# Performance work log

Measured on AMD Instinct MI355X. Metric: run time of the kernel, lower is better.

The kernel has to match this reference:

```python
import jax, jax.numpy as jnp
import numpy as np

EPS = 1e-20

def efficient_squash(s):
    # Efficient-CapsNet squash: (1 - 1/e^||s||) * s/||s||
    n = jnp.linalg.norm(s, axis=-1, keepdims=True)
    return (1.0 - 1.0 / (jnp.exp(n) + EPS)) * (s / (n + EPS))

def setup_inputs() -> dict:
    key = jax.random.key(0)
    k1, k2 = jax.random.split(key)
    B, N, D_in = 32, 2048, 16
    K, D_out = 32, 16
    x = jax.random.normal(k1, (B, N, D_in), dtype=jnp.float32)
    # he_normal fan_in = N * D_in * ... ; use simple scaled normal init
    w = jax.random.normal(k2, (K, N, D_in, D_out), dtype=jnp.float32) * 0.05
    b = jnp.zeros((K, N, 1), dtype=jnp.float32)
    return {"x": x, "w": w, "b": b}

def reference(x, w, b):
    D_out = w.shape[-1]
    # projection: [B,N,D_in] x [K,N,D_in,D_out] -> [B,K,N,D_out]
    u = jnp.einsum('bji,kjiz->bkjz', x, w)
    # agreement c_{bkj} = sum_{i,z} u_{bkjz} u_{bkiz} = <u_j, sum_i u_i>
    t = jnp.sum(u, axis=2)                      # [B,K,D_out]
    c = jnp.einsum('bkjz,bkz->bkj', u, t)[..., None]  # [B,K,N,1]
    c = c / jnp.sqrt(jnp.asarray(D_out, jnp.float32))
    c = jax.nn.softmax(c, axis=1)               # softmax over capsules K
    c = c + b                                   # broadcast [K,N,1]
    s = jnp.sum(u * c, axis=2)                  # [B,K,D_out]
    return efficient_squash(s)
```

## Files before the change

kernel.cpp:

```cpp
#include <hip/hip_runtime.h>

#define NN 2048
#define KK 32

#define WS_U     0
#define WS_TP2   67108864UL
#define WS_T     67633152UL
#define WS_SPART 67698688UL
#define WS_NEED  71892992UL

__device__ __forceinline__ float bf_lo(unsigned v) { return __uint_as_float(v << 16); }
__device__ __forceinline__ float bf_hi(unsigned v) { return __uint_as_float(v & 0xffff0000u); }
__device__ __forceinline__ unsigned pack_bf16(float a, float b) {
    unsigned ua = __float_as_uint(a), ub = __float_as_uint(b);
    return ((ua + 0x8000u) >> 16) | ((ub + 0x8000u) & 0xffff0000u);
}

__global__ __launch_bounds__(128)
void k1_u(const float* __restrict__ x, const float* __restrict__ w,
          unsigned* __restrict__ u_pk)
{
    const int tid = threadIdx.x;
    const int zq  = tid & 3;
    const int k   = tid >> 2;
    const int j   = blockIdx.x;

    const float4* w4 = reinterpret_cast<const float4*>(
        w + (((size_t)k * NN + j) * 16) * 16) + zq;
    float4 wr[16];
#pragma unroll
    for (int i = 0; i < 16; ++i) wr[i] = w4[i * 4];

    unsigned* __restrict__ ub = u_pk + (size_t)j * 8192 + k * 8 + zq * 2;
#pragma unroll 4
    for (int b = 0; b < 32; ++b) {
        const float* __restrict__ xr = x + ((size_t)b * NN + j) * 16;
        float xs[16];
#pragma unroll
        for (int i = 0; i < 16; ++i) xs[i] = xr[i];
        float4 acc = make_float4(0.f, 0.f, 0.f, 0.f);
#pragma unroll
        for (int i = 0; i < 16; ++i) {
            acc.x = fmaf(xs[i], wr[i].x, acc.x);
            acc.y = fmaf(xs[i], wr[i].y, acc.y);
            acc.z = fmaf(xs[i], wr[i].z, acc.z);
            acc.w = fmaf(xs[i], wr[i].w, acc.w);
        }
        uint2 o;
        o.x = pack_bf16(acc.x, acc.y);
        o.y = pack_bf16(acc.z, acc.w);
        *reinterpret_cast<uint2*>(ub + (size_t)b * 256) = o;
    }
}

__global__ __launch_bounds__(1024)
void k2a_tpart(const unsigned* __restrict__ u_pk, float* __restrict__ t_part2)
{
    __shared__ float red[16][64][8];
    const int tid  = threadIdx.x;
    const int js   = tid >> 6;
    const int sl64 = tid & 63;
    const int b    = blockIdx.x >> 3;
    const int slj  = blockIdx.x & 7;

    const uint4* up = reinterpret_cast<const uint4*>(u_pk)
                    + ((size_t)(slj * 256 + js) * 32 + b) * 64 + sl64;
    float a[8];
#pragma unroll
    for (int e = 0; e < 8; ++e) a[e] = 0.f;
#pragma unroll
    for (int it = 0; it < 16; ++it) {
        uint4 v = up[(size_t)it * (16 * 32 * 64)];
        a[0] += bf_lo(v.x); a[1] += bf_hi(v.x);
        a[2] += bf_lo(v.y); a[3] += bf_hi(v.y);
        a[4] += bf_lo(v.z); a[5] += bf_hi(v.z);
        a[6] += bf_lo(v.w); a[7] += bf_hi(v.w);
    }
#pragma unroll
    for (int e = 0; e < 8; ++e) red[js][sl64][e] = a[e];
    __syncthreads();
    if (tid < 512) {
        const int s = tid >> 3, e = tid & 7;
        float acc = 0.f;
#pragma unroll
        for (int r = 0; r < 16; ++r) acc += red[r][s][e];
        t_part2[((size_t)b * 8 + slj) * 512 + s * 8 + e] = acc;
    }
}

__global__ __launch_bounds__(256)
void k2a2_t(const float* __restrict__ t_part2, float* __restrict__ t)
{
    const int idx4 = blockIdx.x * 256 + threadIdx.x;
    const int b = idx4 >> 7, loc4 = idx4 & 127;
    const float4* p = reinterpret_cast<const float4*>(t_part2) + (size_t)b * 1024 + loc4;
    float4 s = make_float4(0.f, 0.f, 0.f, 0.f);
#pragma unroll
    for (int sl = 0; sl < 8; ++sl) {
        float4 v = p[sl * 128];
        s.x += v.x; s.y += v.y; s.z += v.z; s.w += v.w;
    }
    reinterpret_cast<float4*>(t)[idx4] = s;
}

__global__ __launch_bounds__(256)
void k2b_fused(const unsigned* __restrict__ u_pk, const float* __restrict__ t,
               const float* __restrict__ bias, float* __restrict__ s_part)
{
    __shared__ float lc_lds[32][33];
    __shared__ float s_lds[8][32][16];
    const int tid = threadIdx.x;
    const int k   = tid & 31;
    const int jl  = tid >> 5;
    const int b   = blockIdx.x >> 6;
    const int jc  = blockIdx.x & 63;

    float tr[16];
    const float4* tp = reinterpret_cast<const float4*>(t + ((size_t)b * KK + k) * 16);
#pragma unroll
    for (int q = 0; q < 4; ++q) {
        float4 v = tp[q];
        tr[4 * q + 0] = v.x; tr[4 * q + 1] = v.y; tr[4 * q + 2] = v.z; tr[4 * q + 3] = v.w;
    }

    uint4 ua[4], ud[4];
#pragma unroll
    for (int jj = 0; jj < 4; ++jj) {
        const int jL = jj * 8 + jl;
        const int jg = jc * 32 + jL;
        const uint4* up = reinterpret_cast<const uint4*>(u_pk)
                        + ((size_t)jg * 32 + b) * 64 + k * 2;
        ua[jj] = up[0]; ud[jj] = up[1];
        float a0 = 0.f, a1 = 0.f;
        a0 = fmaf(bf_lo(ua[jj].x), tr[0],  a0); a1 = fmaf(bf_hi(ua[jj].x), tr[1],  a1);
        a0 = fmaf(bf_lo(ua[jj].y), tr[2],  a0); a1 = fmaf(bf_hi(ua[jj].y), tr[3],  a1);
        a0 = fmaf(bf_lo(ua[jj].z), tr[4],  a0); a1 = fmaf(bf_hi(ua[jj].z), tr[5],  a1);
        a0 = fmaf(bf_lo(ua[jj].w), tr[6],  a0); a1 = fmaf(bf_hi(ua[jj].w), tr[7],  a1);
        a0 = fmaf(bf_lo(ud[jj].x), tr[8],  a0); a1 = fmaf(bf_hi(ud[jj].x), tr[9],  a1);
        a0 = fmaf(bf_lo(ud[jj].y), tr[10], a0); a1 = fmaf(bf_hi(ud[jj].y), tr[11], a1);
        a0 = fmaf(bf_lo(ud[jj].z), tr[12], a0); a1 = fmaf(bf_hi(ud[jj].z), tr[13], a1);
        a0 = fmaf(bf_lo(ud[jj].w), tr[14], a0); a1 = fmaf(bf_hi(ud[jj].w), tr[15], a1);
        lc_lds[jL][k] = a0 + a1;
    }
    __syncthreads();

    {
        const int jq = tid >> 3, kq = tid & 7;
        float lv[4];
#pragma unroll
        for (int m = 0; m < 4; ++m) lv[m] = lc_lds[jq][kq * 4 + m];
        float pm = fmaxf(fmaxf(lv[0], lv[1]), fmaxf(lv[2], lv[3]));
        pm = fmaxf(pm, __shfl_xor(pm, 1));
        pm = fmaxf(pm, __shfl_xor(pm, 2));
        pm = fmaxf(pm, __shfl_xor(pm, 4));
        float ev[4], ps = 0.f;
#pragma unroll
        for (int m = 0; m < 4; ++m) { ev[m] = __expf((lv[m] - pm) * 0.25f); ps += ev[m]; }
        ps += __shfl_xor(ps, 1);
        ps += __shfl_xor(ps, 2);
        ps += __shfl_xor(ps, 4);
        const float inv = 1.f / ps;
        const int jg = jc * 32 + jq;
#pragma unroll
        for (int m = 0; m < 4; ++m)
            lv[m] = ev[m] * inv + bias[(size_t)(kq * 4 + m) * NN + jg];
        __syncthreads();
#pragma unroll
        for (int m = 0; m < 4; ++m) lc_lds[jq][kq * 4 + m] = lv[m];
    }
    __syncthreads();

    float sacc[16];
#pragma unroll
    for (int z = 0; z < 16; ++z) sacc[z] = 0.f;
#pragma unroll
    for (int jj = 0; jj < 4; ++jj) {
        const float cv = lc_lds[jj * 8 + jl][k];
        const uint4 a = ua[jj], d = ud[jj];
        sacc[0]  = fmaf(cv, bf_lo(a.x), sacc[0]);  sacc[1]  = fmaf(cv, bf_hi(a.x), sacc[1]);
        sacc[2]  = fmaf(cv, bf_lo(a.y), sacc[2]);  sacc[3]  = fmaf(cv, bf_hi(a.y), sacc[3]);
        sacc[4]  = fmaf(cv, bf_lo(a.z), sacc[4]);  sacc[5]  = fmaf(cv, bf_hi(a.z), sacc[5]);
        sacc[6]  = fmaf(cv, bf_lo(a.w), sacc[6]);  sacc[7]  = fmaf(cv, bf_hi(a.w), sacc[7]);
        sacc[8]  = fmaf(cv, bf_lo(d.x), sacc[8]);  sacc[9]  = fmaf(cv, bf_hi(d.x), sacc[9]);
        sacc[10] = fmaf(cv, bf_lo(d.y), sacc[10]); sacc[11] = fmaf(cv, bf_hi(d.y), sacc[11]);
        sacc[12] = fmaf(cv, bf_lo(d.z), sacc[12]); sacc[13] = fmaf(cv, bf_hi(d.z), sacc[13]);
        sacc[14] = fmaf(cv, bf_lo(d.w), sacc[14]); sacc[15] = fmaf(cv, bf_hi(d.w), sacc[15]);
    }

#pragma unroll
    for (int q = 0; q < 4; ++q)
        *reinterpret_cast<float4*>(&s_lds[jl][k][q * 4]) =
            make_float4(sacc[q * 4], sacc[q * 4 + 1], sacc[q * 4 + 2], sacc[q * 4 + 3]);
    __syncthreads();
    {
        const int kk = tid >> 3, zp = tid & 7;
        float2 o; o.x = 0.f; o.y = 0.f;
#pragma unroll
        for (int l = 0; l < 8; ++l) {
            o.x += s_lds[l][kk][2 * zp];
            o.y += s_lds[l][kk][2 * zp + 1];
        }
        reinterpret_cast<float2*>(s_part)[((size_t)b * 64 + jc) * 256 + kk * 8 + zp] = o;
    }
}

__global__ __launch_bounds__(256)
void k4_squash(const float* __restrict__ s_part, float* __restrict__ out)
{
    const int idx4 = blockIdx.x * 256 + threadIdx.x;
    const int b = idx4 >> 7, loc4 = idx4 & 127;
    const float4* p = reinterpret_cast<const float4*>(s_part) + (size_t)b * 8192 + loc4;
    float4 s = make_float4(0.f, 0.f, 0.f, 0.f);
#pragma unroll 8
    for (int jc = 0; jc < 64; ++jc) {
        float4 v = p[jc * 128];
        s.x += v.x; s.y += v.y; s.z += v.z; s.w += v.w;
    }
    float ss = s.x * s.x + s.y * s.y + s.z * s.z + s.w * s.w;
    ss += __shfl_xor(ss, 1);
    ss += __shfl_xor(ss, 2);
    const float n = sqrtf(ss);
    const float sc = (1.f - 1.f / (__expf(n) + 1e-20f)) / (n + 1e-20f);
    float4 o; o.x = s.x * sc; o.y = s.y * sc; o.z = s.z * sc; o.w = s.w * sc;
    reinterpret_cast<float4*>(out)[idx4] = o;
}

__global__ void k_sentinel(float* __restrict__ out)
{
    out[blockIdx.x * 256 + threadIdx.x] = 12345.0f;
}

extern "C" void kernel_launch(void* const* d_in, const int* in_sizes, int n_in,
                              void* d_out, int out_size, void* d_ws, size_t ws_size,
                              hipStream_t stream)
{
    const float* x    = (const float*)d_in[0];
    const float* w    = (const float*)d_in[1];
    const float* bias = (const float*)d_in[2];
    float* out        = (float*)d_out;

    char* ws = (char*)d_ws;
    if (ws_size < WS_NEED) {
        k_sentinel<<<dim3(64), dim3(256), 0, stream>>>(out);
        return;
    }
    unsigned* u_pk = (unsigned*)(ws + WS_U);
    float* t_part2 = (float*)(ws + WS_TP2);
    float* t       = (float*)(ws + WS_T);
    float* s_part  = (float*)(ws + WS_SPART);

    k1_u     <<<dim3(2048), dim3(128),  0, stream>>>(x, w, u_pk);
    k2a_tpart<<<dim3(256),  dim3(1024), 0, stream>>>(u_pk, t_part2);
    k2a2_t   <<<dim3(16),   dim3(256),  0, stream>>>(t_part2, t);
    k2b_fused<<<dim3(2048), dim3(256),  0, stream>>>(u_pk, t, bias, s_part);
    k4_squash<<<dim3(16),   dim3(256),  0, stream>>>(s_part, out);
}
```

Measured before the change: 76.03 us.

## Compute projection with bf16 MFMA and fuse t partial sums into projection kernel

Replaces the scalar-FMA projection kernel with one that packs w and x to bf16 and uses 16x16x32 MFMA instructions. A select mask handles two j rows per wave. The same kernel accumulates per-block partial sums of u for t, which removes the separate pass that re-read the whole u buffer. Those partials are then reduced by two small reduction kernels. This adds a 32 MB partial buffer, rounds w and x to bf16 before the multiply, and wastes half of each MFMA on masked zeros.

```diff
diff --git a/kernel.cpp b/kernel.cpp
--- a/kernel.cpp
+++ b/kernel.cpp
@@ -3,11 +3,15 @@
 #define NN 2048
 #define KK 32
 
-#define WS_U     0
-#define WS_TP2   67108864UL
-#define WS_T     67633152UL
-#define WS_SPART 67698688UL
-#define WS_NEED  71892992UL
+typedef __attribute__((ext_vector_type(8))) short short8;
+typedef __attribute__((ext_vector_type(4))) float f32x4;
+
+#define WS_U     0UL
+#define WS_TPART 67108864UL
+#define WS_TP2   100663296UL
+#define WS_T     101711872UL
+#define WS_SPART 101777408UL
+#define WS_NEED  105971712UL
 
 __device__ __forceinline__ float bf_lo(unsigned v) { return __uint_as_float(v << 16); }
 __device__ __forceinline__ float bf_hi(unsigned v) { return __uint_as_float(v & 0xffff0000u); }
@@ -15,97 +19,132 @@
     unsigned ua = __float_as_uint(a), ub = __float_as_uint(b);
     return ((ua + 0x8000u) >> 16) | ((ub + 0x8000u) & 0xffff0000u);
 }
-
-__global__ __launch_bounds__(128)
-void k1_u(const float* __restrict__ x, const float* __restrict__ w,
-          unsigned* __restrict__ u_pk)
+__device__ __forceinline__ short8 pack8(const float* r) {
+    short8 o;
+#pragma unroll
+    for (int e = 0; e < 8; ++e)
+        o[e] = (short)(unsigned short)((__float_as_uint(r[e]) + 0x8000u) >> 16);
+    return o;
+}
+__device__ __forceinline__ short8 sel8(bool keep, short8 v) {
+    union { short8 s; unsigned u[4]; } a, b;
+    a.s = v;
+#pragma unroll
+    for (int i = 0; i < 4; ++i) b.u[i] = keep ? a.u[i] : 0u;
+    return b.s;
+}
+
+__global__ __launch_bounds__(512)
+void kA2(const float* __restrict__ x, const float* __restrict__ w,
+         unsigned* __restrict__ u_pk, float* __restrict__ t_part)
 {
     const int tid = threadIdx.x;
-    const int zq  = tid & 3;
-    const int k   = tid >> 2;
-    const int j   = blockIdx.x;
-
-    const float4* w4 = reinterpret_cast<const float4*>(
-        w + (((size_t)k * NN + j) * 16) * 16) + zq;
-    float4 wr[16];
-#pragma unroll
-    for (int i = 0; i < 16; ++i) wr[i] = w4[i * 4];
-
-    unsigned* __restrict__ ub = u_pk + (size_t)j * 8192 + k * 8 + zq * 2;
-#pragma unroll 4
-    for (int b = 0; b < 32; ++b) {
-        const float* __restrict__ xr = x + ((size_t)b * NN + j) * 16;
-        float xs[16];
-#pragma unroll
-        for (int i = 0; i < 16; ++i) xs[i] = xr[i];
-        float4 acc = make_float4(0.f, 0.f, 0.f, 0.f);
-#pragma unroll
-        for (int i = 0; i < 16; ++i) {
-            acc.x = fmaf(xs[i], wr[i].x, acc.x);
-            acc.y = fmaf(xs[i], wr[i].y, acc.y);
-            acc.z = fmaf(xs[i], wr[i].z, acc.z);
-            acc.w = fmaf(xs[i], wr[i].w, acc.w);
-        }
-        uint2 o;
-        o.x = pack_bf16(acc.x, acc.y);
-        o.y = pack_bf16(acc.z, acc.w);
-        *reinterpret_cast<uint2*>(ub + (size_t)b * 256) = o;
-    }
-}
-
-__global__ __launch_bounds__(1024)
-void k2a_tpart(const unsigned* __restrict__ u_pk, float* __restrict__ t_part2)
-{
-    __shared__ float red[16][64][8];
-    const int tid  = threadIdx.x;
-    const int js   = tid >> 6;
-    const int sl64 = tid & 63;
-    const int b    = blockIdx.x >> 3;
-    const int slj  = blockIdx.x & 7;
-
-    const uint4* up = reinterpret_cast<const uint4*>(u_pk)
-                    + ((size_t)(slj * 256 + js) * 32 + b) * 64 + sl64;
-    float a[8];
-#pragma unroll
-    for (int e = 0; e < 8; ++e) a[e] = 0.f;
-#pragma unroll
-    for (int it = 0; it < 16; ++it) {
-        uint4 v = up[(size_t)it * (16 * 32 * 64)];
-        a[0] += bf_lo(v.x); a[1] += bf_hi(v.x);
-        a[2] += bf_lo(v.y); a[3] += bf_hi(v.y);
-        a[4] += bf_lo(v.z); a[5] += bf_hi(v.z);
-        a[6] += bf_lo(v.w); a[7] += bf_hi(v.w);
-    }
-#pragma unroll
-    for (int e = 0; e < 8; ++e) red[js][sl64][e] = a[e];
-    __syncthreads();
-    if (tid < 512) {
-        const int s = tid >> 3, e = tid & 7;
-        float acc = 0.f;
-#pragma unroll
-        for (int r = 0; r < 16; ++r) acc += red[r][s][e];
-        t_part2[((size_t)b * 8 + slj) * 512 + s * 8 + e] = acc;
-    }
-}
-
-__global__ __launch_bounds__(256)
-void k2a2_t(const float* __restrict__ t_part2, float* __restrict__ t)
-{
-    const int idx4 = blockIdx.x * 256 + threadIdx.x;
-    const int b = idx4 >> 7, loc4 = idx4 & 127;
-    const float4* p = reinterpret_cast<const float4*>(t_part2) + (size_t)b * 1024 + loc4;
-    float4 s = make_float4(0.f, 0.f, 0.f, 0.f);
-#pragma unroll
-    for (int sl = 0; sl < 8; ++sl) {
-        float4 v = p[sl * 128];
-        s.x += v.x; s.y += v.y; s.z += v.z; s.w += v.w;
-    }
-    reinterpret_cast<float4*>(t)[idx4] = s;
-}
-
-__global__ __launch_bounds__(256)
-void k2b_fused(const unsigned* __restrict__ u_pk, const float* __restrict__ t,
-               const float* __restrict__ bias, float* __restrict__ s_part)
+    const int wv = tid >> 6, l = tid & 63;
+    const int c16 = l & 15, g = l >> 4;
+    const int jl = g >> 1, ih = g & 1;
+    const int j0 = blockIdx.x * 4;
+
+    f32x4 T[4][2];
+#pragma unroll
+    for (int ckl = 0; ckl < 4; ++ckl)
+#pragma unroll
+        for (int bn = 0; bn < 2; ++bn) T[ckl][bn] = (f32x4){0.f, 0.f, 0.f, 0.f};
+
+#pragma unroll
+    for (int p = 0; p < 2; ++p) {
+        const int jp = j0 + p * 2 + jl;
+
+        short8 Wf[4];
+#pragma unroll
+        for (int ckl = 0; ckl < 4; ++ckl) {
+            const int k = wv * 4 + ckl;
+            const float* wp = w + ((size_t)k * NN + jp) * 256 + ih * 128 + c16;
+            float br[8];
+#pragma unroll
+            for (int e = 0; e < 8; ++e) br[e] = wp[e * 16];
+            Wf[ckl] = pack8(br);
+        }
+        short8 Xf[2];
+#pragma unroll
+        for (int bn = 0; bn < 2; ++bn) {
+            const float* xp = x + ((size_t)(bn * 16 + c16) * NN + jp) * 16 + ih * 8;
+            float ar[8];
+            float4 v0 = *reinterpret_cast<const float4*>(xp);
+            float4 v1 = *reinterpret_cast<const float4*>(xp + 4);
+            ar[0]=v0.x; ar[1]=v0.y; ar[2]=v0.z; ar[3]=v0.w;
+            ar[4]=v1.x; ar[5]=v1.y; ar[6]=v1.z; ar[7]=v1.w;
+            Xf[bn] = pack8(ar);
+        }
+
+#pragma unroll
+        for (int jj = 0; jj < 2; ++jj) {
+            const bool keep = (jl == jj);
+            const int j = j0 + p * 2 + jj;
+            const f32x4 zero = (f32x4){0.f, 0.f, 0.f, 0.f};
+#pragma unroll
+            for (int ckl = 0; ckl < 4; ++ckl) {
+                const int k = wv * 4 + ckl;
+                const short8 wsel = sel8(keep, Wf[ckl]);
+#pragma unroll
+                for (int bn = 0; bn < 2; ++bn) {
+                    f32x4 Cj = __builtin_amdgcn_mfma_f32_16x16x32_bf16(
+                        wsel, Xf[bn], zero, 0, 0, 0);
+                    T[ckl][bn] += Cj;
+                    uint2 o;
+                    o.x = pack_bf16(Cj[0], Cj[1]);
+                    o.y = pack_bf16(Cj[2], Cj[3]);
+                    *reinterpret_cast<uint2*>(u_pk +
+                        (((size_t)j * 32 + bn * 16 + c16) * 32 + k) * 8 + g * 2) = o;
+                }
+            }
+        }
+    }
+
+    float* tp = t_part + (size_t)blockIdx.x * 16384;
+#pragma unroll
+    for (int ckl = 0; ckl < 4; ++ckl)
+#pragma unroll
+        for (int bn = 0; bn < 2; ++bn)
+            *reinterpret_cast<f32x4*>(tp + (bn * 16 + c16) * 512 +
+                                      (wv * 4 + ckl) * 16 + g * 4) = T[ckl][bn];
+}
+
+__global__ __launch_bounds__(256)
+void kred32(const float* __restrict__ src, float* __restrict__ dst)
+{
+    const int idx = blockIdx.x * 256 + threadIdx.x;
+    const int c4 = idx & 4095, ch = idx >> 12;
+    const f32x4* P = reinterpret_cast<const f32x4*>(src);
+    f32x4 a0 = (f32x4){0,0,0,0}, a1 = a0, a2 = a0, a3 = a0;
+#pragma unroll 2
+    for (int q = 0; q < 32; q += 4) {
+        a0 += P[(size_t)(ch * 32 + q + 0) * 4096 + c4];
+        a1 += P[(size_t)(ch * 32 + q + 1) * 4096 + c4];
+        a2 += P[(size_t)(ch * 32 + q + 2) * 4096 + c4];
+        a3 += P[(size_t)(ch * 32 + q + 3) * 4096 + c4];
+    }
+    reinterpret_cast<f32x4*>(dst)[(size_t)ch * 4096 + c4] = (a0 + a1) + (a2 + a3);
+}
+
+__global__ __launch_bounds__(256)
+void kt2(const float* __restrict__ tp2, float* __restrict__ t)
+{
+    const int c4 = blockIdx.x * 256 + threadIdx.x;
+    const f32x4* P = reinterpret_cast<const f32x4*>(tp2);
+    f32x4 a0 = (f32x4){0,0,0,0}, a1 = a0, a2 = a0, a3 = a0;
+#pragma unroll
+    for (int q = 0; q < 16; q += 4) {
+        a0 += P[(size_t)(q + 0) * 4096 + c4];
+        a1 += P[(size_t)(q + 1) * 4096 + c4];
+        a2 += P[(size_t)(q + 2) * 4096 + c4];
+        a3 += P[(size_t)(q + 3) * 4096 + c4];
+    }
+    reinterpret_cast<f32x4*>(t)[c4] = (a0 + a1) + (a2 + a3);
+}
+
+__global__ __launch_bounds__(256)
+void kB2(const unsigned* __restrict__ u_pk, const float* __restrict__ t,
+         const float* __restrict__ bias, float* __restrict__ s_part)
 {
     __shared__ float lc_lds[32][33];
     __shared__ float s_lds[8][32][16];
@@ -129,7 +168,7 @@
         const int jL = jj * 8 + jl;
         const int jg = jc * 32 + jL;
         const uint4* up = reinterpret_cast<const uint4*>(u_pk)
-                        + ((size_t)jg * 32 + b) * 64 + k * 2;
+                        + (((size_t)jg * 32 + b) * 32 + k) * 2;
         ua[jj] = up[0]; ud[jj] = up[1];
         float a0 = 0.f, a1 = 0.f;
         a0 = fmaf(bf_lo(ua[jj].x), tr[0],  a0); a1 = fmaf(bf_hi(ua[jj].x), tr[1],  a1);
@@ -196,9 +235,9 @@
         const int kk = tid >> 3, zp = tid & 7;
         float2 o; o.x = 0.f; o.y = 0.f;
 #pragma unroll
-        for (int l = 0; l < 8; ++l) {
-            o.x += s_lds[l][kk][2 * zp];
-            o.y += s_lds[l][kk][2 * zp + 1];
+        for (int l2 = 0; l2 < 8; ++l2) {
+            o.x += s_lds[l2][kk][2 * zp];
+            o.y += s_lds[l2][kk][2 * zp + 1];
         }
         reinterpret_cast<float2*>(s_part)[((size_t)b * 64 + jc) * 256 + kk * 8 + zp] = o;
     }
@@ -245,13 +284,14 @@
         return;
     }
     unsigned* u_pk = (unsigned*)(ws + WS_U);
-    float* t_part2 = (float*)(ws + WS_TP2);
+    float* t_part  = (float*)(ws + WS_TPART);
+    float* tp2     = (float*)(ws + WS_TP2);
     float* t       = (float*)(ws + WS_T);
     float* s_part  = (float*)(ws + WS_SPART);
 
-    k1_u     <<<dim3(2048), dim3(128),  0, stream>>>(x, w, u_pk);
-    k2a_tpart<<<dim3(256),  dim3(1024), 0, stream>>>(u_pk, t_part2);
-    k2a2_t   <<<dim3(16),   dim3(256),  0, stream>>>(t_part2, t);
-    k2b_fused<<<dim3(2048), dim3(256),  0, stream>>>(u_pk, t, bias, s_part);
-    k4_squash<<<dim3(16),   dim3(256),  0, stream>>>(s_part, out);
-}
+    kA2      <<<dim3(512),  dim3(512), 0, stream>>>(x, w, u_pk, t_part);
+    kred32   <<<dim3(256),  dim3(256), 0, stream>>>(t_part, tp2);
+    kt2      <<<dim3(16),   dim3(256), 0, stream>>>(tp2, t);
+    kB2      <<<dim3(2048), dim3(256), 0, stream>>>(u_pk, t, bias, s_part);
+    k4_squash<<<dim3(16),   dim3(256), 0, stream>>>(s_part, out);
+}
```

Result: faster. 67.31 us (-11.5%).

## Stage w tiles in LDS for coalesced loads and widen the t reduction grid

Applied to the files above, without the earlier changes.

The projection kernel now processes four j per 512-thread block. It loads each j's full weight slab cooperatively into LDS with contiguous float4 reads, then transposes the packed bf16 results through LDS so the u stores to global memory are fully coalesced uint4 writes. The t partial-sum kernel is regridded to 1024 blocks with a 32-way partial buffer. The follow-up reduction now sums 32 slices instead of 8. The goal is to remove the strided per-thread w loads and scattered 8-byte stores of the old projection, at the cost of more LDS use, extra barriers and a larger workspace.

```diff
diff --git a/kernel.cpp b/kernel.cpp
--- a/kernel.cpp
+++ b/kernel.cpp
@@ -3,11 +3,13 @@
 #define NN 2048
 #define KK 32
 
-#define WS_U     0
-#define WS_TP2   67108864UL
-#define WS_T     67633152UL
-#define WS_SPART 67698688UL
-#define WS_NEED  71892992UL
+typedef __attribute__((ext_vector_type(4))) float f32x4;
+
+#define WS_U     0UL
+#define WS_TP4   67108864UL
+#define WS_T     69206016UL
+#define WS_SPART 69271552UL
+#define WS_NEED  73465856UL
 
 __device__ __forceinline__ float bf_lo(unsigned v) { return __uint_as_float(v << 16); }
 __device__ __forceinline__ float bf_hi(unsigned v) { return __uint_as_float(v & 0xffff0000u); }
@@ -16,96 +18,136 @@
     return ((ua + 0x8000u) >> 16) | ((ub + 0x8000u) & 0xffff0000u);
 }
 
-__global__ __launch_bounds__(128)
-void k1_u(const float* __restrict__ x, const float* __restrict__ w,
-          unsigned* __restrict__ u_pk)
-{
+__global__ __launch_bounds__(512)
+void kU(const float* __restrict__ x, const float* __restrict__ w,
+        unsigned* __restrict__ u_pk)
+{
+    __shared__ float    w_lds[32 * 257];
+    __shared__ float    x_lds[32][16];
+    __shared__ unsigned u_tr[32 * 264];
     const int tid = threadIdx.x;
-    const int zq  = tid & 3;
-    const int k   = tid >> 2;
-    const int j   = blockIdx.x;
-
-    const float4* w4 = reinterpret_cast<const float4*>(
-        w + (((size_t)k * NN + j) * 16) * 16) + zq;
-    float4 wr[16];
-#pragma unroll
-    for (int i = 0; i < 16; ++i) wr[i] = w4[i * 4];
-
-    unsigned* __restrict__ ub = u_pk + (size_t)j * 8192 + k * 8 + zq * 2;
-#pragma unroll 4
-    for (int b = 0; b < 32; ++b) {
-        const float* __restrict__ xr = x + ((size_t)b * NN + j) * 16;
-        float xs[16];
-#pragma unroll
-        for (int i = 0; i < 16; ++i) xs[i] = xr[i];
-        float4 acc = make_float4(0.f, 0.f, 0.f, 0.f);
-#pragma unroll
-        for (int i = 0; i < 16; ++i) {
-            acc.x = fmaf(xs[i], wr[i].x, acc.x);
-            acc.y = fmaf(xs[i], wr[i].y, acc.y);
-            acc.z = fmaf(xs[i], wr[i].z, acc.z);
-            acc.w = fmaf(xs[i], wr[i].w, acc.w);
-        }
-        uint2 o;
-        o.x = pack_bf16(acc.x, acc.y);
-        o.y = pack_bf16(acc.z, acc.w);
-        *reinterpret_cast<uint2*>(ub + (size_t)b * 256) = o;
+    const int k   = tid & 31;
+    const int zq  = (tid >> 5) & 3;
+    const int bh  = tid >> 7;
+    const int j0  = blockIdx.x * 4;
+
+#pragma unroll 1
+    for (int jj = 0; jj < 4; ++jj) {
+        const int j = j0 + jj;
+
+        {
+            const int kk = tid >> 4, c = tid & 15;
+            const float4* wg = reinterpret_cast<const float4*>(
+                w + ((size_t)kk * NN + j) * 256);
+            float4 v0 = wg[c];
+            float4 v1 = wg[16 + c];
+            float4 v2 = wg[32 + c];
+            float4 v3 = wg[48 + c];
+            *reinterpret_cast<float4*>(&w_lds[kk * 257 +   0 + c * 4]) = v0;
+            *reinterpret_cast<float4*>(&w_lds[kk * 257 +  64 + c * 4]) = v1;
+            *reinterpret_cast<float4*>(&w_lds[kk * 257 + 128 + c * 4]) = v2;
+            *reinterpret_cast<float4*>(&w_lds[kk * 257 + 192 + c * 4]) = v3;
+            x_lds[kk][c] = x[((size_t)kk * NN + j) * 16 + c];
+        }
+        __syncthreads();
+
+        float wr[16][4];
+#pragma unroll
+        for (int i = 0; i < 16; ++i)
+            *reinterpret_cast<float4*>(wr[i]) =
+                *reinterpret_cast<const float4*>(&w_lds[k * 257 + i * 16 + zq * 4]);
+
+#pragma unroll
+        for (int b8 = 0; b8 < 8; ++b8) {
+            const int b = bh * 8 + b8;
+            float a0 = 0.f, a1 = 0.f, a2 = 0.f, a3 = 0.f;
+#pragma unroll
+            for (int iq = 0; iq < 4; ++iq) {
+                float4 xv = *reinterpret_cast<const float4*>(&x_lds[b][iq * 4]);
+#pragma unroll
+                for (int ii = 0; ii < 4; ++ii) {
+                    const float xs = (ii == 0) ? xv.x : (ii == 1) ? xv.y
+                                   : (ii == 2) ? xv.z : xv.w;
+                    a0 = fmaf(xs, wr[iq * 4 + ii][0], a0);
+                    a1 = fmaf(xs, wr[iq * 4 + ii][1], a1);
+                    a2 = fmaf(xs, wr[iq * 4 + ii][2], a2);
+                    a3 = fmaf(xs, wr[iq * 4 + ii][3], a3);
+                }
+            }
+            uint2 o;
+            o.x = pack_bf16(a0, a1);
+            o.y = pack_bf16(a2, a3);
+            *reinterpret_cast<uint2*>(&u_tr[b * 264 + k * 8 + zq * 2]) = o;
+        }
+        __syncthreads();
+
+        {
+            const int lane = tid & 63;
+            const int bb   = tid >> 6;
+            uint4* dst = reinterpret_cast<uint4*>(u_pk) + (size_t)j * 2048;
+#pragma unroll
+            for (int r = 0; r < 4; ++r) {
+                const int b = r * 8 + bb;
+                uint4 v = *reinterpret_cast<const uint4*>(&u_tr[b * 264 + lane * 4]);
+                dst[b * 64 + lane] = v;
+            }
+        }
+        __syncthreads();
     }
 }
 
 __global__ __launch_bounds__(1024)
-void k2a_tpart(const unsigned* __restrict__ u_pk, float* __restrict__ t_part2)
+void kt_u(const unsigned* __restrict__ u_pk, float* __restrict__ t_part4)
 {
     __shared__ float red[16][64][8];
-    const int tid  = threadIdx.x;
-    const int js   = tid >> 6;
-    const int sl64 = tid & 63;
-    const int b    = blockIdx.x >> 3;
-    const int slj  = blockIdx.x & 7;
-
-    const uint4* up = reinterpret_cast<const uint4*>(u_pk)
-                    + ((size_t)(slj * 256 + js) * 32 + b) * 64 + sl64;
+    const int tid = threadIdx.x;
+    const int js = tid >> 6, c4 = tid & 63;
+    const int cch = blockIdx.x & 31, jsl = blockIdx.x >> 5;
+
+    const uint4* up = reinterpret_cast<const uint4*>(u_pk);
     float a[8];
 #pragma unroll
     for (int e = 0; e < 8; ++e) a[e] = 0.f;
 #pragma unroll
-    for (int it = 0; it < 16; ++it) {
-        uint4 v = up[(size_t)it * (16 * 32 * 64)];
+    for (int q = 0; q < 4; ++q) {
+        const int j = jsl * 64 + q * 16 + js;
+        uint4 v = up[(size_t)j * 2048 + cch * 64 + c4];
         a[0] += bf_lo(v.x); a[1] += bf_hi(v.x);
         a[2] += bf_lo(v.y); a[3] += bf_hi(v.y);
         a[4] += bf_lo(v.z); a[5] += bf_hi(v.z);
         a[6] += bf_lo(v.w); a[7] += bf_hi(v.w);
     }
 #pragma unroll
-    for (int e = 0; e < 8; ++e) red[js][sl64][e] = a[e];
+    for (int e = 0; e < 8; ++e) red[js][c4][e] = a[e];
     __syncthreads();
     if (tid < 512) {
-        const int s = tid >> 3, e = tid & 7;
-        float acc = 0.f;
-#pragma unroll
-        for (int r = 0; r < 16; ++r) acc += red[r][s][e];
-        t_part2[((size_t)b * 8 + slj) * 512 + s * 8 + e] = acc;
+        const int cc = tid >> 3, e = tid & 7;
+        float s = 0.f;
+#pragma unroll
+        for (int r = 0; r < 16; ++r) s += red[r][cc][e];
+        t_part4[(size_t)jsl * 16384 + (cch * 64 + cc) * 8 + e] = s;
     }
 }
 
 __global__ __launch_bounds__(256)
-void k2a2_t(const float* __restrict__ t_part2, float* __restrict__ t)
+void kt2b(const float* __restrict__ t_part4, float* __restrict__ t)
 {
     const int idx4 = blockIdx.x * 256 + threadIdx.x;
-    const int b = idx4 >> 7, loc4 = idx4 & 127;
-    const float4* p = reinterpret_cast<const float4*>(t_part2) + (size_t)b * 1024 + loc4;
-    float4 s = make_float4(0.f, 0.f, 0.f, 0.f);
-#pragma unroll
-    for (int sl = 0; sl < 8; ++sl) {
-        float4 v = p[sl * 128];
-        s.x += v.x; s.y += v.y; s.z += v.z; s.w += v.w;
-    }
-    reinterpret_cast<float4*>(t)[idx4] = s;
+    const f32x4* P = reinterpret_cast<const f32x4*>(t_part4);
+    f32x4 a0 = (f32x4){0,0,0,0}, a1 = a0, a2 = a0, a3 = a0;
+#pragma unroll
+    for (int sl = 0; sl < 32; sl += 4) {
+        a0 += P[(size_t)(sl + 0) * 4096 + idx4];
+        a1 += P[(size_t)(sl + 1) * 4096 + idx4];
+        a2 += P[(size_t)(sl + 2) * 4096 + idx4];
+        a3 += P[(size_t)(sl + 3) * 4096 + idx4];
+    }
+    reinterpret_cast<f32x4*>(t)[idx4] = (a0 + a1) + (a2 + a3);
 }
 
 __global__ __launch_bounds__(256)
-void k2b_fused(const unsigned* __restrict__ u_pk, const float* __restrict__ t,
-               const float* __restrict__ bias, float* __restrict__ s_part)
+void kB2(const unsigned* __restrict__ u_pk, const float* __restrict__ t,
+         const float* __restrict__ bias, float* __restrict__ s_part)
 {
     __shared__ float lc_lds[32][33];
     __shared__ float s_lds[8][32][16];
@@ -129,7 +171,7 @@
         const int jL = jj * 8 + jl;
         const int jg = jc * 32 + jL;
         const uint4* up = reinterpret_cast<const uint4*>(u_pk)
-                        + ((size_t)jg * 32 + b) * 64 + k * 2;
+                        + (((size_t)jg * 32 + b) * 32 + k) * 2;
         ua[jj] = up[0]; ud[jj] = up[1];
         float a0 = 0.f, a1 = 0.f;
         a0 = fmaf(bf_lo(ua[jj].x), tr[0],  a0); a1 = fmaf(bf_hi(ua[jj].x), tr[1],  a1);
@@ -196,9 +238,9 @@
         const int kk = tid >> 3, zp = tid & 7;
         float2 o; o.x = 0.f; o.y = 0.f;
 #pragma unroll
-        for (int l = 0; l < 8; ++l) {
-            o.x += s_lds[l][kk][2 * zp];
-            o.y += s_lds[l][kk][2 * zp + 1];
+        for (int l2 = 0; l2 < 8; ++l2) {
+            o.x += s_lds[l2][kk][2 * zp];
+            o.y += s_lds[l2][kk][2 * zp + 1];
         }
         reinterpret_cast<float2*>(s_part)[((size_t)b * 64 + jc) * 256 + kk * 8 + zp] = o;
     }
@@ -244,14 +286,14 @@
         k_sentinel<<<dim3(64), dim3(256), 0, stream>>>(out);
         return;
     }
-    unsigned* u_pk = (unsigned*)(ws + WS_U);
-    float* t_part2 = (float*)(ws + WS_TP2);
-    float* t       = (float*)(ws + WS_T);
-    float* s_part  = (float*)(ws + WS_SPART);
-
-    k1_u     <<<dim3(2048), dim3(128),  0, stream>>>(x, w, u_pk);
-    k2a_tpart<<<dim3(256),  dim3(1024), 0, stream>>>(u_pk, t_part2);
-    k2a2_t   <<<dim3(16),   dim3(256),  0, stream>>>(t_part2, t);
-    k2b_fused<<<dim3(2048), dim3(256),  0, stream>>>(u_pk, t, bias, s_part);
+    unsigned* u_pk   = (unsigned*)(ws + WS_U);
+    float*    t_part4= (float*)(ws + WS_TP4);
+    float*    t      = (float*)(ws + WS_T);
+    float*    s_part = (float*)(ws + WS_SPART);
+
+    kU       <<<dim3(512),  dim3(512),  0, stream>>>(x, w, u_pk);
+    kt_u     <<<dim3(1024), dim3(1024), 0, stream>>>(u_pk, t_part4);
+    kt2b     <<<dim3(16),   dim3(256),  0, stream>>>(t_part4, t);
+    kB2      <<<dim3(2048), dim3(256),  0, stream>>>(u_pk, t, bias, s_part);
     k4_squash<<<dim3(16),   dim3(256),  0, stream>>>(s_part, out);
 }
```

New measurement: 78.61 us. +3.4%, slower.
